# Kernel tuning notes

Hardware: AMD Instinct MI355X
Metric: run time of the kernel (lower is better)

The kernel has to match this reference:

```python
import jax, jax.numpy as jnp
import numpy as np

N = 50000      # total nodes
E = 800000     # edges (before self loops)
B = 512        # graphs in batch
NODE_F = 9
GLOB_F = 4
IN_F = 13
H = 4          # heads
C = 16         # per-head channels (64 // 4)
HID = 64
NEG_SLOPE = 0.2


def setup_inputs() -> dict:
    key = jax.random.key(0)
    ks = jax.random.split(key, 32)
    inp = {}
    inp["node_feats"] = jax.random.normal(ks[0], (N, NODE_F), jnp.float32)
    inp["x_global_features"] = jax.random.normal(ks[1], (B, GLOB_F), jnp.float32)
    inp["edge_index"] = jax.random.randint(ks[2], (2, E), 0, N, jnp.int32)
    inp["batch_idx"] = jnp.sort(jax.random.randint(ks[3], (N,), 0, B, jnp.int32))
    dims = [IN_F, HID, HID]
    k = 4
    for l in range(3):
        s = 1.0 / np.sqrt(dims[l])
        inp[f"W{l}"] = jax.random.normal(ks[k], (dims[l], H * C), jnp.float32) * s; k += 1
        inp[f"att_src{l}"] = jax.random.normal(ks[k], (H, C), jnp.float32) * 0.1; k += 1
        inp[f"att_dst{l}"] = jax.random.normal(ks[k], (H, C), jnp.float32) * 0.1; k += 1
        inp[f"b{l}"] = jnp.zeros((H * C,), jnp.float32)
    mlp_dims = [(64, 64), (64, 64), (64, 64), (64, 1)]
    for i, (a, o) in enumerate(mlp_dims):
        inp[f"mlp_W{i}"] = jax.random.normal(ks[k], (a, o), jnp.float32) * (1.0 / np.sqrt(a)); k += 1
        inp[f"mlp_b{i}"] = jnp.zeros((o,), jnp.float32)
    return inp


def _gat_conv(x, src, dst, W, a_src, a_dst, bias, n):
    # h: [n, H, C]
    h = (x @ W).reshape(n, H, C)
    alpha_src = jnp.sum(h * a_src, axis=-1)   # [n, H]
    alpha_dst = jnp.sum(h * a_dst, axis=-1)   # [n, H]
    e = alpha_src[src] + alpha_dst[dst]       # [E', H]
    e = jax.nn.leaky_relu(e, NEG_SLOPE)
    # softmax over incoming edges per destination node (self loops guarantee >=1 edge)
    m = jax.ops.segment_max(e, dst, num_segments=n)
    e = jnp.exp(e - m[dst])
    s = jax.ops.segment_sum(e, dst, num_segments=n)
    alpha = e / s[dst]                        # [E', H]
    out = jax.ops.segment_sum(h[src] * alpha[:, :, None], dst, num_segments=n)
    return out.reshape(n, H * C) + bias


def _forward(node_feats, x_global_features,
             W0, att_src0, att_dst0, b0,
             W1, att_src1, att_dst1, b1,
             W2, att_src2, att_dst2, b2,
             mlp_W0, mlp_b0, mlp_W1, mlp_b1, mlp_W2, mlp_b2, mlp_W3, mlp_b3,
             edge_index, batch_idx):
    n = node_feats.shape[0]
    # concat per-graph global features onto each node
    x = jnp.concatenate([node_feats, x_global_features[batch_idx]], axis=1)  # [N, 13]
    loops = jnp.arange(n, dtype=edge_index.dtype)
    src = jnp.concatenate([edge_index[0], loops])
    dst = jnp.concatenate([edge_index[1], loops])
    x = jax.nn.relu(_gat_conv(x, src, dst, W0, att_src0, att_dst0, b0, n))
    x = jax.nn.relu(_gat_conv(x, src, dst, W1, att_src1, att_dst1, b1, n))
    x = _gat_conv(x, src, dst, W2, att_src2, att_dst2, b2, n)  # no act on last layer
    # scatter_mean over graphs
    sums = jax.ops.segment_sum(x, batch_idx, num_segments=B)
    cnt = jax.ops.segment_sum(jnp.ones((n,), x.dtype), batch_idx, num_segments=B)
    pooled = sums / jnp.clip(cnt, 1.0)[:, None]               # [B, 64]
    h = jax.nn.relu(pooled @ mlp_W0 + mlp_b0)
    h = jax.nn.relu(h @ mlp_W1 + mlp_b1)
    h = jax.nn.relu(h @ mlp_W2 + mlp_b2)
    out = h @ mlp_W3 + mlp_b3                                  # [B, 1]
    return out.reshape(-1)                                     # flatten -> [B]


def reference(node_feats, x_global_features,
              W0, att_src0, att_dst0, b0,
              W1, att_src1, att_dst1, b1,
              W2, att_src2, att_dst2, b2,
              mlp_W0, mlp_b0, mlp_W1, mlp_b1, mlp_W2, mlp_b2, mlp_W3, mlp_b3,
              edge_index, batch_idx):
    return _forward(node_feats, x_global_features,
                    W0, att_src0, att_dst0, b0,
                    W1, att_src1, att_dst1, b1,
                    W2, att_src2, att_dst2, b2,
                    mlp_W0, mlp_b0, mlp_W1, mlp_b1, mlp_W2, mlp_b2, mlp_W3, mlp_b3,
                    edge_index, batch_idx)
```

## Files before the change

kernel.cpp:

```cpp
#include <hip/hip_runtime.h>
#include <hip/hip_fp16.h>

#define GAT_H 4
#define GAT_HC 64
#define NEG_SLOPE 0.2f
#define DB 128
#define NBMAX 512
#define CHUNK 4096
#define EPT 16

__device__ __forceinline__ float lrelu(float x) { return x >= 0.f ? x : NEG_SLOPE * x; }

template <int K, bool CONCAT>
__global__ __launch_bounds__(256) void gemm_attn(
    const float* __restrict__ x, const float* __restrict__ nf,
    const float* __restrict__ gf, const int* __restrict__ batch,
    const float* __restrict__ W,
    const float* __restrict__ att_s, const float* __restrict__ att_d,
    __half* __restrict__ h, float* __restrict__ asrc, float* __restrict__ adst,
    int N, int nwaves)
{
    int lane = threadIdx.x & 63;
    int wid = blockIdx.x * 4 + __builtin_amdgcn_readfirstlane(threadIdx.x >> 6);

    float w[K];
    #pragma unroll
    for (int k = 0; k < K; ++k) w[k] = W[k * 64 + lane];
    float as_c = att_s[lane];
    float ad_c = att_d[lane];

    for (int row = wid; row < N; row += nwaves) {
        float acc = 0.f;
        if (CONCAT) {
            #pragma unroll
            for (int k = 0; k < 9; ++k) acc = fmaf(nf[row * 9 + k], w[k], acc);
            int b = batch[row];
            #pragma unroll
            for (int k = 0; k < 4; ++k) acc = fmaf(gf[b * 4 + k], w[9 + k], acc);
        } else {
            #pragma unroll
            for (int k = 0; k < K; ++k) acc = fmaf(x[(size_t)row * K + k], w[k], acc);
        }
        h[(unsigned)row * 64u + (unsigned)lane] = __float2half(acc);
        float vs = acc * as_c;
        float vd = acc * ad_c;
        #pragma unroll
        for (int off = 8; off; off >>= 1) { vs += __shfl_xor(vs, off); vd += __shfl_xor(vd, off); }
        if ((lane & 15) == 0) {
            asrc[row * GAT_H + (lane >> 4)] = vs;
            adst[row * GAT_H + (lane >> 4)] = vd;
        }
    }
}


__global__ __launch_bounds__(256) void zero_small(unsigned* __restrict__ bin_cnt,
                                                  unsigned* __restrict__ bin_fill)
{
    int t = threadIdx.x;
    bin_cnt[t] = 0; bin_cnt[t + 256] = 0;
    bin_fill[t] = 0; bin_fill[t + 256] = 0;
}

__global__ __launch_bounds__(256) void hist_bins(const int* __restrict__ dst,
                                                 unsigned* __restrict__ bin_cnt, int E)
{
    __shared__ unsigned lh[NBMAX];
    int t = threadIdx.x;
    lh[t] = 0; lh[t + 256] = 0;
    __syncthreads();
    for (int e = blockIdx.x * 256 + t; e < E; e += gridDim.x * 256)
        atomicAdd(&lh[((unsigned)dst[e]) >> 7], 1u);
    __syncthreads();
    unsigned v = lh[t];       if (v) atomicAdd(&bin_cnt[t], v);
    v = lh[t + 256];          if (v) atomicAdd(&bin_cnt[t + 256], v);
}

__global__ __launch_bounds__(256) void scan_bins(const unsigned* __restrict__ bin_cnt,
                                                 unsigned* __restrict__ bin_base,
                                                 int* __restrict__ indptr,
                                                 int nb, int N, int E)
{
    __shared__ unsigned buf[NBMAX];
    int t = threadIdx.x;
    buf[t] = (t < nb) ? bin_cnt[t] : 0u;
    buf[t + 256] = (t + 256 < nb) ? bin_cnt[t + 256] : 0u;
    __syncthreads();
    for (int off = 1; off < NBMAX; off <<= 1) {
        unsigned a = 0, b = 0;
        if (t >= off) a = buf[t - off];
        b = buf[t + 256 - off];
        __syncthreads();
        buf[t] += a; buf[t + 256] += b;
        __syncthreads();
    }
    if (t == 0) { bin_base[0] = 0; indptr[N] = E; }
    if (t < nb) bin_base[t + 1] = buf[t];
    if (t + 256 < nb) bin_base[t + 257] = buf[t + 256];
}

__global__ __launch_bounds__(256) void bin_scatter(const int* __restrict__ src,
                                                   const int* __restrict__ dst,
                                                   const unsigned* __restrict__ bin_base,
                                                   unsigned* __restrict__ bin_fill,
                                                   unsigned* __restrict__ binned, int E)
{
    __shared__ unsigned lh[NBMAX];
    __shared__ int goff[NBMAX];
    __shared__ unsigned sorted[CHUNK];
    int t = threadIdx.x;
    lh[t] = 0; lh[t + 256] = 0;
    __syncthreads();
    int e0 = blockIdx.x * CHUNK;

    unsigned pk[EPT]; int bn[EPT]; unsigned rk[EPT];
    #pragma unroll
    for (int i = 0; i < EPT; ++i) {
        int e = e0 + i * 256 + t;
        bn[i] = -1;
        if (e < E) {
            unsigned d = (unsigned)dst[e];
            pk[i] = (d << 16) | (unsigned)src[e];
            bn[i] = (int)(d >> 7);
            rk[i] = atomicAdd(&lh[bn[i]], 1u);
        }
    }
    __syncthreads();
    unsigned c0 = lh[t], c1 = lh[t + 256];
    for (int off = 1; off < NBMAX; off <<= 1) {
        unsigned a = 0, b = 0;
        if (t >= off) a = lh[t - off];
        b = lh[t + 256 - off];
        __syncthreads();
        lh[t] += a; lh[t + 256] += b;
        __syncthreads();
    }
    unsigned x0 = lh[t] - c0, x1 = lh[t + 256] - c1;
    if (c0) { unsigned g = atomicAdd(&bin_fill[t], c0);
              goff[t] = (int)(bin_base[t] + g) - (int)x0; }
    if (c1) { unsigned g = atomicAdd(&bin_fill[t + 256], c1);
              goff[t + 256] = (int)(bin_base[t + 256] + g) - (int)x1; }
    lh[t] = x0; lh[t + 256] = x1;
    __syncthreads();
    #pragma unroll
    for (int i = 0; i < EPT; ++i)
        if (bn[i] >= 0) sorted[lh[bn[i]] + rk[i]] = pk[i];
    __syncthreads();
    int T = min(CHUNK, E - e0);
    for (int j = t; j < T; j += 256) {
        unsigned p = sorted[j];
        binned[goff[p >> 23] + j] = p;
    }
}

__global__ __launch_bounds__(256) void bin_finalize(const unsigned* __restrict__ binned,
                                                    const unsigned* __restrict__ bin_base,
                                                    int* __restrict__ csr_src,
                                                    int* __restrict__ indptr, int N)
{
    __shared__ unsigned lh[DB];
    __shared__ unsigned fill[DB];
    int t = threadIdx.x, b = blockIdx.x;
    unsigned base = bin_base[b];
    unsigned cnt = bin_base[b + 1] - base;
    if (t < DB) lh[t] = 0;
    __syncthreads();
    for (unsigned i = t; i < cnt; i += 256)
        atomicAdd(&lh[(binned[base + i] >> 16) & (DB - 1)], 1u);
    __syncthreads();
    unsigned c0 = (t < DB) ? lh[t] : 0;
    for (int off = 1; off < DB; off <<= 1) {
        unsigned a = 0;
        if (t >= off && t < DB) a = lh[t - off];
        __syncthreads();
        if (t < DB) lh[t] += a;
        __syncthreads();
    }
    if (t < DB) {
        unsigned excl = lh[t] - c0;
        int d = b * DB + t;
        if (d < N) indptr[d] = (int)(base + excl);
        fill[t] = excl;
    }
    __syncthreads();
    for (unsigned i = t; i < cnt; i += 256) {
        unsigned p = binned[base + i];
        unsigned pos = atomicAdd(&fill[(p >> 16) & (DB - 1)], 1u);
        csr_src[base + pos] = (int)(p & 0xFFFFu);
    }
}

template <bool RELU>
__global__ __launch_bounds__(256) void aggregate(
    const __half* __restrict__ h, const float* __restrict__ asrc,
    const float* __restrict__ adst, const int* __restrict__ indptr,
    const int* __restrict__ csr_src, const float* __restrict__ bias,
    float* __restrict__ xout, int N, int nwaves)
{
    int lane = threadIdx.x & 63;
    int wid = blockIdx.x * 4 + __builtin_amdgcn_readfirstlane(threadIdx.x >> 6);
    unsigned h16 = (unsigned)(lane >> 4);
    float bias_c = bias[lane];

    for (int node = wid; node < N; node += nwaves) {
        int beg = __builtin_amdgcn_readfirstlane(indptr[node]);
        int end = __builtin_amdgcn_readfirstlane(indptr[node + 1]);
        unsigned un = (unsigned)node;

        float adst_n = adst[un * 4u + h16];
        float p0 = __expf(lrelu(asrc[un * 4u + h16] + adst_n));
        float sacc = p0;
        float acc = __half2float(h[un * 64u + (unsigned)lane]) * p0;

        int e = beg;
        for (; e + 8 <= end; e += 8) {
            int s[8]; float a[8], hv[8];
            #pragma unroll
            for (int i = 0; i < 8; ++i) s[i] = csr_src[e + i];
            #pragma unroll
            for (int i = 0; i < 8; ++i) a[i] = asrc[(unsigned)s[i] * 4u + h16];
            #pragma unroll
            for (int i = 0; i < 8; ++i)
                hv[i] = __half2float(h[(unsigned)s[i] * 64u + (unsigned)lane]);
            #pragma unroll
            for (int i = 0; i < 8; ++i) {
                float p = __expf(lrelu(a[i] + adst_n));
                sacc += p;
                acc = fmaf(hv[i], p, acc);
            }
        }
        for (; e + 2 <= end; e += 2) {
            int s0 = csr_src[e], s1 = csr_src[e + 1];
            float a0 = asrc[(unsigned)s0 * 4u + h16];
            float a1 = asrc[(unsigned)s1 * 4u + h16];
            float h0 = __half2float(h[(unsigned)s0 * 64u + (unsigned)lane]);
            float h1 = __half2float(h[(unsigned)s1 * 64u + (unsigned)lane]);
            float pa = __expf(lrelu(a0 + adst_n));
            float pb = __expf(lrelu(a1 + adst_n));
            sacc += pa + pb;
            acc = fmaf(h0, pa, acc);
            acc = fmaf(h1, pb, acc);
        }
        if (e < end) {
            int s = csr_src[e];
            float p = __expf(lrelu(asrc[(unsigned)s * 4u + h16] + adst_n));
            sacc += p;
            acc = fmaf(__half2float(h[(unsigned)s * 64u + (unsigned)lane]), p, acc);
        }

        float o = acc / sacc + bias_c;
        if (RELU) o = fmaxf(o, 0.f);
        xout[un * 64u + (unsigned)lane] = o;
    }
}

__global__ void pool_mlp(const float* __restrict__ x, const int* __restrict__ batch, int N,
                         const float* __restrict__ W0, const float* __restrict__ b0,
                         const float* __restrict__ W1, const float* __restrict__ b1,
                         const float* __restrict__ W2, const float* __restrict__ b2,
                         const float* __restrict__ W3, const float* __restrict__ b3,
                         float* __restrict__ out)
{
    __shared__ int bounds[2];
    __shared__ float red[4][64];
    __shared__ float hb[64];
    int b = blockIdx.x, t = threadIdx.x;

    if (t < 2) {
        int target = b + t;
        int lo = 0, hi = N;
        while (lo < hi) {
            int mid = (lo + hi) >> 1;
            if (batch[mid] < target) lo = mid + 1; else hi = mid;
        }
        bounds[t] = lo;
    }
    __syncthreads();
    int beg = bounds[0], end = bounds[1];

    int c = t & 63, w = t >> 6;
    float sum = 0.f;
    for (int n = beg + w; n < end; n += 4) sum += x[(size_t)n * 64 + c];
    red[w][c] = sum;
    __syncthreads();
    if (t < 64) {
        float v = red[0][t] + red[1][t] + red[2][t] + red[3][t];
        float cb = fmaxf((float)(end - beg), 1.0f);
        hb[t] = v / cb;
    }
    __syncthreads();

    float v0 = 0.f;
    if (t < 64) {
        v0 = b0[t];
        for (int k = 0; k < 64; ++k) v0 = fmaf(hb[k], W0[k * 64 + t], v0);
        v0 = fmaxf(v0, 0.f);
    }
    __syncthreads(); if (t < 64) hb[t] = v0; __syncthreads();
    if (t < 64) {
        v0 = b1[t];
        for (int k = 0; k < 64; ++k) v0 = fmaf(hb[k], W1[k * 64 + t], v0);
        v0 = fmaxf(v0, 0.f);
    }
    __syncthreads(); if (t < 64) hb[t] = v0; __syncthreads();
    if (t < 64) {
        v0 = b2[t];
        for (int k = 0; k < 64; ++k) v0 = fmaf(hb[k], W2[k * 64 + t], v0);
        v0 = fmaxf(v0, 0.f);
    }
    __syncthreads(); if (t < 64) hb[t] = v0; __syncthreads();
    if (t < 64) {
        float r = hb[t] * W3[t];
        #pragma unroll
        for (int off = 32; off; off >>= 1) r += __shfl_xor(r, off);
        if (t == 0) out[b] = r + b3[0];
    }
}

extern "C" void kernel_launch(void* const* d_in, const int* in_sizes, int n_in,
                              void* d_out, int out_size, void* d_ws, size_t ws_size,
                              hipStream_t stream)
{
    const float* node_feats = (const float*)d_in[0];
    const float* glob       = (const float*)d_in[1];
    const int*   edge_index = (const int*)d_in[2];
    const int*   batch      = (const int*)d_in[3];
    const float* W[3]  = {(const float*)d_in[4],  (const float*)d_in[8],  (const float*)d_in[12]};
    const float* As[3] = {(const float*)d_in[5],  (const float*)d_in[9],  (const float*)d_in[13]};
    const float* Ad[3] = {(const float*)d_in[6],  (const float*)d_in[10], (const float*)d_in[14]};
    const float* Bi[3] = {(const float*)d_in[7],  (const float*)d_in[11], (const float*)d_in[15]};
    const float* mW0 = (const float*)d_in[16]; const float* mb0 = (const float*)d_in[17];
    const float* mW1 = (const float*)d_in[18]; const float* mb1 = (const float*)d_in[19];
    const float* mW2 = (const float*)d_in[20]; const float* mb2 = (const float*)d_in[21];
    const float* mW3 = (const float*)d_in[22]; const float* mb3 = (const float*)d_in[23];
    float* out = (float*)d_out;

    int N = in_sizes[0] / 9;
    int E = in_sizes[2] / 2;
    int B = in_sizes[1] / 4;
    const int* esrc = edge_index;
    const int* edst = edge_index + E;
    int nb = (N + DB - 1) / DB;

    char* ws = (char*)d_ws;
    size_t off = 0;
    auto alloc = [&](size_t bytes) -> void* {
        void* p = ws + off;
        off = (off + bytes + 255) & ~(size_t)255;
        return p;
    };
    __half*   hbuf     = (__half*)alloc((size_t)N * 64 * 2);
    float*    xbuf     = (float*)alloc((size_t)N * 64 * 4);
    float*    asrc     = (float*)alloc((size_t)N * GAT_H * 4);
    float*    adst     = (float*)alloc((size_t)N * GAT_H * 4);
    int*      indptr   = (int*)alloc((size_t)(N + 1) * 4);
    int*      csr_src  = (int*)alloc((size_t)E * 4);
    unsigned* binned   = (unsigned*)alloc((size_t)E * 4);
    unsigned* bin_cnt  = (unsigned*)alloc(NBMAX * 4);
    unsigned* bin_base = (unsigned*)alloc((NBMAX + 1) * 4);
    unsigned* bin_fill = (unsigned*)alloc(NBMAX * 4);
    (void)ws_size;

    zero_small<<<1, 256, 0, stream>>>(bin_cnt, bin_fill);
    hist_bins<<<400, 256, 0, stream>>>(edst, bin_cnt, E);
    scan_bins<<<1, 256, 0, stream>>>(bin_cnt, bin_base, indptr, nb, N, E);
    bin_scatter<<<(E + CHUNK - 1) / CHUNK, 256, 0, stream>>>(esrc, edst, bin_base, bin_fill,
                                                             binned, E);
    bin_finalize<<<nb, 256, 0, stream>>>(binned, bin_base, csr_src, indptr, N);

    const int gemmBlocks = 1024;
    const int aggBlocks = 6250;
    gemm_attn<13, true><<<gemmBlocks, 256, 0, stream>>>(nullptr, node_feats, glob, batch,
                                                        W[0], As[0], Ad[0], hbuf, asrc, adst,
                                                        N, gemmBlocks * 4);
    aggregate<true><<<aggBlocks, 256, 0, stream>>>(hbuf, asrc, adst, indptr, csr_src, Bi[0],
                                                   xbuf, N, aggBlocks * 4);
    gemm_attn<64, false><<<gemmBlocks, 256, 0, stream>>>(xbuf, nullptr, nullptr, nullptr,
                                                         W[1], As[1], Ad[1], hbuf, asrc, adst,
                                                         N, gemmBlocks * 4);
    aggregate<true><<<aggBlocks, 256, 0, stream>>>(hbuf, asrc, adst, indptr, csr_src, Bi[1],
                                                   xbuf, N, aggBlocks * 4);
    gemm_attn<64, false><<<gemmBlocks, 256, 0, stream>>>(xbuf, nullptr, nullptr, nullptr,
                                                         W[2], As[2], Ad[2], hbuf, asrc, adst,
                                                         N, gemmBlocks * 4);
    aggregate<false><<<aggBlocks, 256, 0, stream>>>(hbuf, asrc, adst, indptr, csr_src, Bi[2],
                                                    xbuf, N, aggBlocks * 4);

    pool_mlp<<<B, 256, 0, stream>>>(xbuf, batch, N,
                                    mW0, mb0, mW1, mb1, mW2, mb2, mW3, mb3, out);
}
```

Baseline: 188.4 us.

## Parallelize GAT aggregation across edges within a wavefront with vector loads

Restructures the aggregate kernel so each wavefront handles 16 incoming edges at once: each group of four lanes covers one edge, one lane per head, and loads that head's 16 half channels with 128-bit loads. Partial sums are combined with xor shuffles, and one lane group writes float4 outputs. This replaces the serial per-edge loop over all 64 lanes, which depended on long load latency chains. The cost is a 16-register accumulator array plus a shuffle reduction per node, and the aggregate grid is doubled to 12500 blocks so every node gets its own wave.

```diff
diff --git a/kernel.cpp b/kernel.cpp
--- a/kernel.cpp
+++ b/kernel.cpp
@@ -199,58 +199,74 @@
 {
     int lane = threadIdx.x & 63;
     int wid = blockIdx.x * 4 + __builtin_amdgcn_readfirstlane(threadIdx.x >> 6);
-    unsigned h16 = (unsigned)(lane >> 4);
-    float bias_c = bias[lane];
+    int eslot = lane >> 2;
+    unsigned s = (unsigned)(lane & 3);
+
+    float4 bias_r[4];
+    #pragma unroll
+    for (int c = 0; c < 4; ++c)
+        bias_r[c] = reinterpret_cast<const float4*>(bias)[s * 4u + c];
 
     for (int node = wid; node < N; node += nwaves) {
         int beg = __builtin_amdgcn_readfirstlane(indptr[node]);
         int end = __builtin_amdgcn_readfirstlane(indptr[node + 1]);
-        unsigned un = (unsigned)node;
-
-        float adst_n = adst[un * 4u + h16];
-        float p0 = __expf(lrelu(asrc[un * 4u + h16] + adst_n));
-        float sacc = p0;
-        float acc = __half2float(h[un * 64u + (unsigned)lane]) * p0;
-
-        int e = beg;
-        for (; e + 8 <= end; e += 8) {
-            int s[8]; float a[8], hv[8];
+        int total = (end - beg) + 1;
+
+        float adst_n = adst[(unsigned)node * 4u + s];
+        float sacc = 0.f;
+        float acc[16];
+        #pragma unroll
+        for (int i = 0; i < 16; ++i) acc[i] = 0.f;
+
+        for (int g0 = 0; g0 < total; g0 += 16) {
+            int idx = g0 + eslot;
+            if (idx < total) {
+                int src = (idx == 0) ? node : csr_src[beg + idx - 1];
+                float a = asrc[(unsigned)src * 4u + s];
+                const uint4* hp =
+                    reinterpret_cast<const uint4*>(h + (unsigned)src * 64u + s * 16u);
+                uint4 hv0 = hp[0];
+                uint4 hv1 = hp[1];
+                float p = __expf(lrelu(a + adst_n));
+                sacc += p;
+                const __half2* hh0 = reinterpret_cast<const __half2*>(&hv0);
+                const __half2* hh1 = reinterpret_cast<const __half2*>(&hv1);
+                #pragma unroll
+                for (int j = 0; j < 4; ++j) {
+                    float2 f0 = __half22float2(hh0[j]);
+                    acc[j * 2 + 0] = fmaf(f0.x, p, acc[j * 2 + 0]);
+                    acc[j * 2 + 1] = fmaf(f0.y, p, acc[j * 2 + 1]);
+                    float2 f1 = __half22float2(hh1[j]);
+                    acc[8 + j * 2 + 0] = fmaf(f1.x, p, acc[8 + j * 2 + 0]);
+                    acc[8 + j * 2 + 1] = fmaf(f1.y, p, acc[8 + j * 2 + 1]);
+                }
+            }
+        }
+
+        #pragma unroll
+        for (int off = 4; off <= 32; off <<= 1) {
+            sacc += __shfl_xor(sacc, off);
             #pragma unroll
-            for (int i = 0; i < 8; ++i) s[i] = csr_src[e + i];
+            for (int i = 0; i < 16; ++i) acc[i] += __shfl_xor(acc[i], off);
+        }
+
+        if (eslot == 0) {
+            float inv = 1.0f / sacc;
+            float4* op = reinterpret_cast<float4*>(xout + (unsigned)node * 64u + s * 16u);
             #pragma unroll
-            for (int i = 0; i < 8; ++i) a[i] = asrc[(unsigned)s[i] * 4u + h16];
-            #pragma unroll
-            for (int i = 0; i < 8; ++i)
-                hv[i] = __half2float(h[(unsigned)s[i] * 64u + (unsigned)lane]);
-            #pragma unroll
-            for (int i = 0; i < 8; ++i) {
-                float p = __expf(lrelu(a[i] + adst_n));
-                sacc += p;
-                acc = fmaf(hv[i], p, acc);
+            for (int c = 0; c < 4; ++c) {
+                float4 o;
+                o.x = fmaf(acc[c * 4 + 0], inv, bias_r[c].x);
+                o.y = fmaf(acc[c * 4 + 1], inv, bias_r[c].y);
+                o.z = fmaf(acc[c * 4 + 2], inv, bias_r[c].z);
+                o.w = fmaf(acc[c * 4 + 3], inv, bias_r[c].w);
+                if (RELU) {
+                    o.x = fmaxf(o.x, 0.f); o.y = fmaxf(o.y, 0.f);
+                    o.z = fmaxf(o.z, 0.f); o.w = fmaxf(o.w, 0.f);
+                }
+                op[c] = o;
             }
         }
-        for (; e + 2 <= end; e += 2) {
-            int s0 = csr_src[e], s1 = csr_src[e + 1];
-            float a0 = asrc[(unsigned)s0 * 4u + h16];
-            float a1 = asrc[(unsigned)s1 * 4u + h16];
-            float h0 = __half2float(h[(unsigned)s0 * 64u + (unsigned)lane]);
-            float h1 = __half2float(h[(unsigned)s1 * 64u + (unsigned)lane]);
-            float pa = __expf(lrelu(a0 + adst_n));
-            float pb = __expf(lrelu(a1 + adst_n));
-            sacc += pa + pb;
-            acc = fmaf(h0, pa, acc);
-            acc = fmaf(h1, pb, acc);
-        }
-        if (e < end) {
-            int s = csr_src[e];
-            float p = __expf(lrelu(asrc[(unsigned)s * 4u + h16] + adst_n));
-            sacc += p;
-            acc = fmaf(__half2float(h[(unsigned)s * 64u + (unsigned)lane]), p, acc);
-        }
-
-        float o = acc / sacc + bias_c;
-        if (RELU) o = fmaxf(o, 0.f);
-        xout[un * 64u + (unsigned)lane] = o;
     }
 }
 
@@ -369,7 +385,7 @@
     bin_finalize<<<nb, 256, 0, stream>>>(binned, bin_base, csr_src, indptr, N);
 
     const int gemmBlocks = 1024;
-    const int aggBlocks = 6250;
+    const int aggBlocks = 12500;
     gemm_attn<13, true><<<gemmBlocks, 256, 0, stream>>>(nullptr, node_feats, glob, batch,
                                                         W[0], As[0], Ad[0], hbuf, asrc, adst,
                                                         N, gemmBlocks * 4);
```

Result: slower. 231.6 us (+22.9%).

## Compute attention weights cooperatively per edge batch and drop zeroing kernel

Applied to the files above, without the earlier changes.

The aggregation kernel is restructured so each wave computes the attention exponentials for 16 edges across all 4 heads at once, one edge-head pair per lane. It then broadcasts the weights with shuffles while gathering features, so each exp is computed once instead of redundantly per channel lane. The log2(e) factor is folded into the attention vectors so exp2f can replace expf. The histogram now writes per-block slices that the scan kernel reduces, which removes the zeroing kernel launch and the global atomics. The CSR array is padded so tail reads stay in bounds, and the aggregation grid is doubled, adding shuffle overhead and padded-lane work.

```diff
diff --git a/kernel.cpp b/kernel.cpp
--- a/kernel.cpp
+++ b/kernel.cpp
@@ -4,10 +4,12 @@
 #define GAT_H 4
 #define GAT_HC 64
 #define NEG_SLOPE 0.2f
+#define LOG2E 1.4426950408889634f
 #define DB 128
 #define NBMAX 512
 #define CHUNK 4096
 #define EPT 16
+#define SLICES 128
 
 __device__ __forceinline__ float lrelu(float x) { return x >= 0.f ? x : NEG_SLOPE * x; }
 
@@ -26,8 +28,8 @@
     float w[K];
     #pragma unroll
     for (int k = 0; k < K; ++k) w[k] = W[k * 64 + lane];
-    float as_c = att_s[lane];
-    float ad_c = att_d[lane];
+    float as_c = att_s[lane] * LOG2E;
+    float ad_c = att_d[lane] * LOG2E;
 
     for (int row = wid; row < N; row += nwaves) {
         float acc = 0.f;
@@ -54,16 +56,8 @@
 }
 
 
-__global__ __launch_bounds__(256) void zero_small(unsigned* __restrict__ bin_cnt,
-                                                  unsigned* __restrict__ bin_fill)
-{
-    int t = threadIdx.x;
-    bin_cnt[t] = 0; bin_cnt[t + 256] = 0;
-    bin_fill[t] = 0; bin_fill[t + 256] = 0;
-}
-
 __global__ __launch_bounds__(256) void hist_bins(const int* __restrict__ dst,
-                                                 unsigned* __restrict__ bin_cnt, int E)
+                                                 unsigned* __restrict__ slices, int E)
 {
     __shared__ unsigned lh[NBMAX];
     int t = threadIdx.x;
@@ -72,19 +66,26 @@
     for (int e = blockIdx.x * 256 + t; e < E; e += gridDim.x * 256)
         atomicAdd(&lh[((unsigned)dst[e]) >> 7], 1u);
     __syncthreads();
-    unsigned v = lh[t];       if (v) atomicAdd(&bin_cnt[t], v);
-    v = lh[t + 256];          if (v) atomicAdd(&bin_cnt[t + 256], v);
-}
-
-__global__ __launch_bounds__(256) void scan_bins(const unsigned* __restrict__ bin_cnt,
+    unsigned* slice = slices + (size_t)blockIdx.x * NBMAX;
+    slice[t] = lh[t];
+    slice[t + 256] = lh[t + 256];
+}
+
+__global__ __launch_bounds__(256) void scan_bins(const unsigned* __restrict__ slices,
                                                  unsigned* __restrict__ bin_base,
+                                                 unsigned* __restrict__ bin_fill,
                                                  int* __restrict__ indptr,
-                                                 int nb, int N, int E)
+                                                 int nslices, int N, int E)
 {
     __shared__ unsigned buf[NBMAX];
     int t = threadIdx.x;
-    buf[t] = (t < nb) ? bin_cnt[t] : 0u;
-    buf[t + 256] = (t + 256 < nb) ? bin_cnt[t + 256] : 0u;
+    unsigned s0 = 0, s1 = 0;
+    for (int s = 0; s < nslices; ++s) {
+        s0 += slices[(size_t)s * NBMAX + t];
+        s1 += slices[(size_t)s * NBMAX + t + 256];
+    }
+    buf[t] = s0; buf[t + 256] = s1;
+    bin_fill[t] = 0; bin_fill[t + 256] = 0;
     __syncthreads();
     for (int off = 1; off < NBMAX; off <<= 1) {
         unsigned a = 0, b = 0;
@@ -95,8 +96,8 @@
         __syncthreads();
     }
     if (t == 0) { bin_base[0] = 0; indptr[N] = E; }
-    if (t < nb) bin_base[t + 1] = buf[t];
-    if (t + 256 < nb) bin_base[t + 257] = buf[t + 256];
+    bin_base[t + 1] = buf[t];
+    bin_base[t + 257] = buf[t + 256];
 }
 
 __global__ __launch_bounds__(256) void bin_scatter(const int* __restrict__ src,
@@ -156,11 +157,12 @@
 __global__ __launch_bounds__(256) void bin_finalize(const unsigned* __restrict__ binned,
                                                     const unsigned* __restrict__ bin_base,
                                                     int* __restrict__ csr_src,
-                                                    int* __restrict__ indptr, int N)
+                                                    int* __restrict__ indptr, int N, int E)
 {
     __shared__ unsigned lh[DB];
     __shared__ unsigned fill[DB];
     int t = threadIdx.x, b = blockIdx.x;
+    if (b == 0 && t < 16) csr_src[E + t] = 0;
     unsigned base = bin_base[b];
     unsigned cnt = bin_base[b + 1] - base;
     if (t < DB) lh[t] = 0;
@@ -191,7 +193,7 @@
 }
 
 template <bool RELU>
-__global__ __launch_bounds__(256) void aggregate(
+__global__ __launch_bounds__(256) void aggregate3(
     const __half* __restrict__ h, const float* __restrict__ asrc,
     const float* __restrict__ adst, const int* __restrict__ indptr,
     const int* __restrict__ csr_src, const float* __restrict__ bias,
@@ -199,55 +201,52 @@
 {
     int lane = threadIdx.x & 63;
     int wid = blockIdx.x * 4 + __builtin_amdgcn_readfirstlane(threadIdx.x >> 6);
-    unsigned h16 = (unsigned)(lane >> 4);
+    int h16 = lane >> 4;
+    unsigned hp = (unsigned)(lane & 3);
+    int el = lane >> 2;
     float bias_c = bias[lane];
 
     for (int node = wid; node < N; node += nwaves) {
         int beg = __builtin_amdgcn_readfirstlane(indptr[node]);
         int end = __builtin_amdgcn_readfirstlane(indptr[node + 1]);
+        int cnt = end - beg;
         unsigned un = (unsigned)node;
 
-        float adst_n = adst[un * 4u + h16];
-        float p0 = __expf(lrelu(asrc[un * 4u + h16] + adst_n));
-        float sacc = p0;
+        float p0 = exp2f(lrelu(asrc[un * 4u + (unsigned)h16] + adst[un * 4u + (unsigned)h16]));
         float acc = __half2float(h[un * 64u + (unsigned)lane]) * p0;
-
-        int e = beg;
-        for (; e + 8 <= end; e += 8) {
-            int s[8]; float a[8], hv[8];
+        float adst_p = adst[un * 4u + hp];
+        float sacc_p = 0.f;
+
+        for (int g = 0; g < cnt; g += 16) {
+            int idx = beg + g + el;
+            float a = (g + el < cnt) ? asrc[(unsigned)csr_src[idx] * 4u + hp]
+                                     : -INFINITY;
+            float p = exp2f(lrelu(a + adst_p));
+            float ps = p;
+            ps += __shfl_xor(ps, 4);
+            ps += __shfl_xor(ps, 8);
+            ps += __shfl_xor(ps, 16);
+            ps += __shfl_xor(ps, 32);
+            sacc_p += ps;
+
             #pragma unroll
-            for (int i = 0; i < 8; ++i) s[i] = csr_src[e + i];
-            #pragma unroll
-            for (int i = 0; i < 8; ++i) a[i] = asrc[(unsigned)s[i] * 4u + h16];
-            #pragma unroll
-            for (int i = 0; i < 8; ++i)
-                hv[i] = __half2float(h[(unsigned)s[i] * 64u + (unsigned)lane]);
-            #pragma unroll
-            for (int i = 0; i < 8; ++i) {
-                float p = __expf(lrelu(a[i] + adst_n));
-                sacc += p;
-                acc = fmaf(hv[i], p, acc);
+            for (int sb = 0; sb < 2; ++sb) {
+                if (g + sb * 8 >= cnt) break;
+                int base = beg + g + sb * 8;
+                __half hv[8]; float pe[8];
+                #pragma unroll
+                for (int i = 0; i < 8; ++i) {
+                    int s = csr_src[base + i];
+                    hv[i] = h[(unsigned)s * 64u + (unsigned)lane];
+                    pe[i] = __shfl(p, (sb * 8 + i) * 4 + h16);
+                }
+                #pragma unroll
+                for (int i = 0; i < 8; ++i)
+                    acc = fmaf(__half2float(hv[i]), pe[i], acc);
             }
         }
-        for (; e + 2 <= end; e += 2) {
-            int s0 = csr_src[e], s1 = csr_src[e + 1];
-            float a0 = asrc[(unsigned)s0 * 4u + h16];
-            float a1 = asrc[(unsigned)s1 * 4u + h16];
-            float h0 = __half2float(h[(unsigned)s0 * 64u + (unsigned)lane]);
-            float h1 = __half2float(h[(unsigned)s1 * 64u + (unsigned)lane]);
-            float pa = __expf(lrelu(a0 + adst_n));
-            float pb = __expf(lrelu(a1 + adst_n));
-            sacc += pa + pb;
-            acc = fmaf(h0, pa, acc);
-            acc = fmaf(h1, pb, acc);
-        }
-        if (e < end) {
-            int s = csr_src[e];
-            float p = __expf(lrelu(asrc[(unsigned)s * 4u + h16] + adst_n));
-            sacc += p;
-            acc = fmaf(__half2float(h[(unsigned)s * 64u + (unsigned)lane]), p, acc);
-        }
-
+
+        float sacc = p0 + __shfl(sacc_p, h16);
         float o = acc / sacc + bias_c;
         if (RELU) o = fmaxf(o, 0.f);
         xout[un * 64u + (unsigned)lane] = o;
@@ -354,37 +353,36 @@
     float*    asrc     = (float*)alloc((size_t)N * GAT_H * 4);
     float*    adst     = (float*)alloc((size_t)N * GAT_H * 4);
     int*      indptr   = (int*)alloc((size_t)(N + 1) * 4);
-    int*      csr_src  = (int*)alloc((size_t)E * 4);
+    int*      csr_src  = (int*)alloc((size_t)(E + 16) * 4);
     unsigned* binned   = (unsigned*)alloc((size_t)E * 4);
-    unsigned* bin_cnt  = (unsigned*)alloc(NBMAX * 4);
+    unsigned* slices   = (unsigned*)alloc((size_t)SLICES * NBMAX * 4);
     unsigned* bin_base = (unsigned*)alloc((NBMAX + 1) * 4);
     unsigned* bin_fill = (unsigned*)alloc(NBMAX * 4);
     (void)ws_size;
 
-    zero_small<<<1, 256, 0, stream>>>(bin_cnt, bin_fill);
-    hist_bins<<<400, 256, 0, stream>>>(edst, bin_cnt, E);
-    scan_bins<<<1, 256, 0, stream>>>(bin_cnt, bin_base, indptr, nb, N, E);
+    hist_bins<<<SLICES, 256, 0, stream>>>(edst, slices, E);
+    scan_bins<<<1, 256, 0, stream>>>(slices, bin_base, bin_fill, indptr, SLICES, N, E);
     bin_scatter<<<(E + CHUNK - 1) / CHUNK, 256, 0, stream>>>(esrc, edst, bin_base, bin_fill,
                                                              binned, E);
-    bin_finalize<<<nb, 256, 0, stream>>>(binned, bin_base, csr_src, indptr, N);
+    bin_finalize<<<nb, 256, 0, stream>>>(binned, bin_base, csr_src, indptr, N, E);
 
     const int gemmBlocks = 1024;
-    const int aggBlocks = 6250;
+    const int aggBlocks = 12500;
     gemm_attn<13, true><<<gemmBlocks, 256, 0, stream>>>(nullptr, node_feats, glob, batch,
                                                         W[0], As[0], Ad[0], hbuf, asrc, adst,
                                                         N, gemmBlocks * 4);
-    aggregate<true><<<aggBlocks, 256, 0, stream>>>(hbuf, asrc, adst, indptr, csr_src, Bi[0],
-                                                   xbuf, N, aggBlocks * 4);
+    aggregate3<true><<<aggBlocks, 256, 0, stream>>>(hbuf, asrc, adst, indptr, csr_src, Bi[0],
+                                                    xbuf, N, aggBlocks * 4);
     gemm_attn<64, false><<<gemmBlocks, 256, 0, stream>>>(xbuf, nullptr, nullptr, nullptr,
                                                          W[1], As[1], Ad[1], hbuf, asrc, adst,
                                                          N, gemmBlocks * 4);
-    aggregate<true><<<aggBlocks, 256, 0, stream>>>(hbuf, asrc, adst, indptr, csr_src, Bi[1],
-                                                   xbuf, N, aggBlocks * 4);
+    aggregate3<true><<<aggBlocks, 256, 0, stream>>>(hbuf, asrc, adst, indptr, csr_src, Bi[1],
+                                                    xbuf, N, aggBlocks * 4);
     gemm_attn<64, false><<<gemmBlocks, 256, 0, stream>>>(xbuf, nullptr, nullptr, nullptr,
                                                          W[2], As[2], Ad[2], hbuf, asrc, adst,
                                                          N, gemmBlocks * 4);
-    aggregate<false><<<aggBlocks, 256, 0, stream>>>(hbuf, asrc, adst, indptr, csr_src, Bi[2],
-                                                    xbuf, N, aggBlocks * 4);
+    aggregate3<false><<<aggBlocks, 256, 0, stream>>>(hbuf, asrc, adst, indptr, csr_src, Bi[2],
+                                                     xbuf, N, aggBlocks * 4);
 
     pool_mlp<<<B, 256, 0, stream>>>(xbuf, batch, N,
                                     mW0, mb0, mW1, mb1, mW2, mb2, mW3, mb3, out);
```

Result: slower. 194.5 us (+3.2%).
